# Kernel tuning notes

Hardware: AMD Instinct MI355X
Metric: run time of the kernel (lower is better)

The kernel has to match this reference:

```python
import jax, jax.numpy as jnp
import numpy as np

B, SQ, SKV, DIN, DOUT = 8, 2048, 2048, 512, 512

def setup_inputs() -> dict:
    key = jax.random.key(0)
    ks = jax.random.split(key, 8)
    s = 1.0 / np.sqrt(DIN)
    return {
        "query": jax.random.normal(ks[0], (B, SQ, DIN), jnp.float32),
        "key": jax.random.normal(ks[1], (B, SKV, DIN), jnp.float32),
        "value": jax.random.normal(ks[2], (B, SKV, DIN), jnp.float32),
        "offset": jax.random.normal(ks[3], (B, SQ, DIN), jnp.float32),
        "Wq": jax.random.normal(ks[4], (DIN, DOUT), jnp.float32) * s,
        "Wk": jax.random.normal(ks[5], (DIN, DOUT), jnp.float32) * s,
        "Wv": jax.random.normal(ks[6], (DIN, DOUT), jnp.float32) * s,
        "Woff": jax.random.normal(ks[7], (DIN, SKV), jnp.float32) * s,
    }

def reference(query, key, value, offset, Wq, Wk, Wv, Woff):
    # q/k/v projections (nn.Linear, no bias)
    q = jnp.einsum("bqi,io->bqo", query, Wq)   # [B,SQ,DOUT]
    k = jnp.einsum("bki,io->bko", key, Wk)     # [B,SKV,DOUT]
    v = jnp.einsum("bki,io->bko", value, Wv)   # [B,SKV,DOUT]
    scale = 1.0 / jnp.sqrt(jnp.asarray(q.shape[-1], jnp.float32))
    scores = jnp.einsum("bqd,bkd->bqk", q, k) * scale  # [B,SQ,SKV]
    attn = jax.nn.softmax(scores, axis=-1)
    # offset bias is added AFTER softmax (no renormalization), per original
    attn = attn + jnp.einsum("bqi,ik->bqk", offset, Woff)
    return jnp.einsum("bqk,bkd->bqd", attn, v)  # [B,SQ,DOUT]
```

## Files before the change

kernel.cpp:

```cpp
#include <hip/hip_runtime.h>
#include <hip/hip_bf16.h>
#include <stdint.h>

typedef __bf16 bf16;
typedef unsigned char u8;
typedef bf16 bf16x4_t __attribute__((ext_vector_type(4)));
typedef bf16 bf16x8_t __attribute__((ext_vector_type(8)));
typedef float floatx4_t __attribute__((ext_vector_type(4)));

#define NB 8
#define SQ 2048
#define SKV 2048
#define DIN 512
#define DOUT 512

#define SCORE_SCALE 0.0027621358640099513f
#define P_STORE_SCALE 0.0625f
#define P_UNDO_SCALE 16.0f

__device__ __forceinline__ void load_lds16(const void* g, void* l) {
    __builtin_amdgcn_global_load_lds(
        (const __attribute__((address_space(1))) unsigned int*)g,
        (__attribute__((address_space(3))) unsigned int*)l, 16, 0, 0);
}

__device__ __forceinline__ u8 to_fp8(float f) {
    int v = __builtin_amdgcn_cvt_pk_fp8_f32(f, 0.f, 0, false);
    return (u8)(v & 0xff);
}
__device__ __forceinline__ unsigned int pack_fp8x4(float a, float b, float c, float d) {
    int lo = __builtin_amdgcn_cvt_pk_fp8_f32(a, b, 0, false);
    int all = __builtin_amdgcn_cvt_pk_fp8_f32(c, d, lo, true);
    return (unsigned int)all;
}

__device__ __forceinline__ int swz_off(int row, int col) {
    return (col & ~63) | ((((col >> 4) & 3) ^ ((row >> 1) & 3)) << 4) | (col & 15);
}

__device__ __forceinline__ void cast_bf16_16B(const float4* s4, u8* d, int t, int rs) {
    const long long b0 = (long long)t * 16;
    const int row = (int)(b0 >> rs);
    const int cb = (int)(b0 & ((1 << rs) - 1));
    float4 f0 = s4[t * 2], f1 = s4[t * 2 + 1];
    bf16x8_t o = { (bf16)f0.x, (bf16)f0.y, (bf16)f0.z, (bf16)f0.w,
                   (bf16)f1.x, (bf16)f1.y, (bf16)f1.z, (bf16)f1.w };
    *(bf16x8_t*)&d[((long long)row << rs) + swz_off(row, cb)] = o;
}

struct CastArgs {
    const float* src[3];
    void* dst[3];
    int n[3];
    int mode[3];
    int rowshift[3];
};
__global__ __launch_bounds__(256) void cast_many(CastArgs a) {
    const int z = blockIdx.z;
    const int t = blockIdx.x * 256 + threadIdx.x;
    if (t >= a.n[z]) return;
    const float4* s4 = (const float4*)a.src[z];
    u8* d = (u8*)a.dst[z];
    const int rs = a.rowshift[z];
    if (a.mode[z] == 1) {
        const long long b0 = (long long)t * 16;
        const int row = (int)(b0 >> rs);
        const int cb = (int)(b0 & ((1 << rs) - 1));
        u8* dst = &d[((long long)row << rs) + swz_off(row, cb)];
        float4 f[4];
#pragma unroll
        for (int k = 0; k < 4; ++k) f[k] = s4[t * 4 + k];
        uint4 o;
        o.x = pack_fp8x4(f[0].x, f[0].y, f[0].z, f[0].w);
        o.y = pack_fp8x4(f[1].x, f[1].y, f[1].z, f[1].w);
        o.z = pack_fp8x4(f[2].x, f[2].y, f[2].z, f[2].w);
        o.w = pack_fp8x4(f[3].x, f[3].y, f[3].z, f[3].w);
        *(uint4*)dst = o;
    } else {
        cast_bf16_16B(s4, d, t, rs);
    }
}

struct TWArgs { const float* src[3]; void* dst[3]; };
__global__ void transpose_w(TWArgs a) {
    __shared__ float t[32][33];
    const float* src = a.src[blockIdx.z];
    int tx = threadIdx.x, ty = threadIdx.y;
    int x0 = blockIdx.x * 32, y0 = blockIdx.y * 32;
#pragma unroll
    for (int j = 0; j < 4; ++j)
        t[ty + 8 * j][tx] = src[(y0 + ty + 8 * j) * DIN + x0 + tx];
    __syncthreads();
    if (blockIdx.z <= 1) {
        u8* d8 = (u8*)a.dst[blockIdx.z];
#pragma unroll
        for (int j = 0; j < 4; ++j) {
            int row = x0 + ty + 8 * j, col = y0 + tx;
            d8[row * 512 + swz_off(row, col)] = to_fp8(t[tx][ty + 8 * j] * 4.0f);
        }
    } else {
        u8* db = (u8*)a.dst[2];
#pragma unroll
        for (int j = 0; j < 4; ++j) {
            int row = x0 + ty + 8 * j, cb = (y0 + tx) * 2;
            *(bf16*)&db[(long long)row * 1024 + swz_off(row, cb)] = (bf16)t[tx][ty + 8 * j];
        }
    }
}

__device__ __forceinline__ void gemm_mainloop(
    floatx4_t (&acc)[4][4], const bf16* __restrict__ Ap, const bf16* __restrict__ Bp,
    int lda, int ldb, int K, bf16* As, bf16* Bs, int wave, int lane)
{
    const int wm = (wave & 1) * 64, wn = (wave >> 1) * 64;
    const int lm = lane & 15, quad = lane >> 4;
    const int srow = lane >> 2, scol = (lane & 3) * 8;
    const int key = (lm >> 1) & 3;

    auto STAGE = [&](int buf, int k0) {
#pragma unroll
        for (int t = 0; t < 2; ++t) {
            const int r0 = (wave * 2 + t) * 16;
            load_lds16(Ap + (long long)(r0 + srow) * lda + (k0 + scol),
                       &As[buf * 4096 + r0 * 32]);
            load_lds16(Bp + (long long)(r0 + srow) * ldb + (k0 + scol),
                       &Bs[buf * 4096 + r0 * 32]);
        }
    };

    STAGE(0, 0);
    __syncthreads();
    int cur = 0;
    for (int k0 = 0; k0 < K; k0 += 32) {
        if (k0 + 32 < K) STAGE(cur ^ 1, k0 + 32);
        bf16x8_t af[4], bfr[4];
#pragma unroll
        for (int i = 0; i < 4; ++i)
            af[i] = *(const bf16x8_t*)&As[cur * 4096 + (wm + i * 16 + lm) * 32 + (quad ^ key) * 8];
#pragma unroll
        for (int i = 0; i < 4; ++i)
            bfr[i] = *(const bf16x8_t*)&Bs[cur * 4096 + (wn + i * 16 + lm) * 32 + (quad ^ key) * 8];
#pragma unroll
        for (int i = 0; i < 4; ++i)
#pragma unroll
            for (int j = 0; j < 4; ++j)
                acc[i][j] = __builtin_amdgcn_mfma_f32_16x16x32_bf16(af[i], bfr[j], acc[i][j], 0, 0, 0);
        __syncthreads();
        cur ^= 1;
    }
}

__device__ __forceinline__ void gemm_mainloop_fp8(
    floatx4_t (&acc)[4][4], const u8* __restrict__ Ap, const u8* __restrict__ Bp,
    int lda, int ldb, int K, u8* As, u8* Bs, int wave, int lane)
{
    const int wm = (wave & 1) * 64, wn = (wave >> 1) * 64;
    const int lm = lane & 15, quad = lane >> 4;
    const int srow = lane >> 2, scol = (lane & 3) * 16;
    const int key = (lm >> 1) & 3;
    const int inner = (quad & 1) * 8;
    const int gh = quad >> 1;

    auto STAGE = [&](int buf, int k0) {
#pragma unroll
        for (int t = 0; t < 2; ++t) {
            const int r0 = (wave * 2 + t) * 16;
            load_lds16(Ap + (long long)(r0 + srow) * lda + k0 + scol, &As[buf * 8192 + r0 * 64]);
            load_lds16(Bp + (long long)(r0 + srow) * ldb + k0 + scol, &Bs[buf * 8192 + r0 * 64]);
        }
    };

    STAGE(0, 0);
    __syncthreads();
    int cur = 0;
    for (int k0 = 0; k0 < K; k0 += 64) {
        if (k0 + 64 < K) STAGE(cur ^ 1, k0 + 64);
#pragma unroll
        for (int p = 0; p < 2; ++p) {
            const int gL = p * 2 + gh;
            const int koff = ((gL ^ key) << 4) + inner;
            long long a[4], b[4];
#pragma unroll
            for (int i = 0; i < 4; ++i)
                a[i] = *(const long long*)&As[cur * 8192 + (wm + i * 16 + lm) * 64 + koff];
#pragma unroll
            for (int i = 0; i < 4; ++i)
                b[i] = *(const long long*)&Bs[cur * 8192 + (wn + i * 16 + lm) * 64 + koff];
#pragma unroll
            for (int i = 0; i < 4; ++i)
#pragma unroll
                for (int j = 0; j < 4; ++j)
                    acc[i][j] = __builtin_amdgcn_mfma_f32_16x16x32_fp8_fp8(a[i], b[j], acc[i][j], 0, 0, 0);
        }
        __syncthreads();
        cur ^= 1;
    }
}

__global__ __launch_bounds__(256) void proj_gemm(
    const u8* __restrict__ query8, const u8* __restrict__ key8,
    const u8* __restrict__ WqT8, const u8* __restrict__ WkT8,
    u8* __restrict__ Qb8, u8* __restrict__ Kb8,
    const bf16* __restrict__ valueb, const bf16* __restrict__ WvT,
    bf16* __restrict__ VT, u8* __restrict__ VT8,
    const float* __restrict__ Woff, bf16* __restrict__ Woffb)
{
    __shared__ __align__(16) u8 smem[32768];
    const int tid = threadIdx.x;
    const int id = blockIdx.x;
    if (id >= 1536) {
        const int t = (id - 1536) * 256 + tid;
        cast_bf16_16B((const float4*)Woff, (u8*)Woffb, t, 12);
        return;
    }
    const int wave = tid >> 6, lane = tid & 63;
    const int wm = (wave & 1) * 64, wn = (wave >> 1) * 64;
    const int lm = lane & 15, quad = lane >> 4;

    floatx4_t acc[4][4];
#pragma unroll
    for (int i = 0; i < 4; ++i)
#pragma unroll
        for (int j = 0; j < 4; ++j) acc[i][j] = 0.0f;

    if (id < 1024) {
        const int xcd = id & 7, t = id >> 3, m = t & 3;
        const int gg = xcd + 8 * (t >> 2);
        const int y = gg & 127, z = gg >> 7;
        const u8* Ap = (z ? key8 : query8) + (long long)y * 128 * DIN;
        const u8* Bp = (z ? WkT8 : WqT8) + (long long)m * 128 * DIN;
        gemm_mainloop_fp8(acc, Ap, Bp, DIN, DIN, DIN, smem, smem + 16384, wave, lane);
        u8* C = z ? Kb8 : Qb8;
#pragma unroll
        for (int i = 0; i < 4; ++i)
#pragma unroll
            for (int j = 0; j < 4; ++j) {
                const int row0 = y * 128 + wm + i * 16 + quad * 4;
                const int col = m * 128 + wn + j * 16 + lm;
#pragma unroll
                for (int r = 0; r < 4; ++r)
                    C[(long long)(row0 + r) * DOUT + swz_off(row0 + r, col)] = to_fp8(acc[i][j][r]);
            }
    } else {
        const int id2 = id - 1024;
        const int z = id2 & 7, r2 = id2 >> 3;
        const int ym = r2 & 3, xn = r2 >> 2;
        const bf16* Ap = WvT + (long long)ym * 128 * DIN;
        const bf16* Bp = valueb + (long long)z * (SKV * DIN) + (long long)xn * 128 * DIN;
        gemm_mainloop(acc, Ap, Bp, DIN, DIN, DIN, (bf16*)smem, (bf16*)(smem + 16384), wave, lane);
        u8* C = (u8*)(VT + (long long)z * (DOUT * SKV));
        u8* C8 = VT8 + (long long)z * (DOUT * SKV);
#pragma unroll
        for (int i = 0; i < 4; ++i)
#pragma unroll
            for (int j = 0; j < 4; ++j) {
                const int row0 = ym * 128 + wm + i * 16 + quad * 4;
                const int col = xn * 128 + wn + j * 16 + lm;
#pragma unroll
                for (int r = 0; r < 4; ++r) {
                    float v = acc[i][j][r];
                    const int rr = row0 + r;
                    *(bf16*)&C[(long long)rr * (SKV * 2) + swz_off(rr, col * 2)] = (bf16)v;
                    C8[(long long)rr * SKV + swz_off(rr, col)] = to_fp8(v);
                }
            }
    }
}

__global__ __launch_bounds__(256) void g_gemm(
    const bf16* __restrict__ VT, const bf16* __restrict__ Woffb,
    float* __restrict__ G32a, float* __restrict__ G32b,
    const float* __restrict__ offset, bf16* __restrict__ offsetb,
    float* __restrict__ lbuf)
{
    __shared__ __align__(16) u8 smem[32768];
    const int tid = threadIdx.x;
    const int id = blockIdx.x;
    if (id >= 4352) {
        float4* d4 = (float4*)lbuf;
        const int t = (id - 4352) * 256 + tid;
#pragma unroll
        for (int k = 0; k < 4; ++k)
            d4[t * 4 + k] = make_float4(0.f, 0.f, 0.f, 0.f);
        return;
    }
    if (id >= 256) {
        const int t = (id - 256) * 256 + tid;
        cast_bf16_16B((const float4*)offset, (u8*)offsetb, t, 10);
        return;
    }
    const int wave = tid >> 6, lane = tid & 63;
    const int z = id & 7, h = (id >> 3) & 1, x = (id >> 4) & 3, y = (id >> 6) & 3;

    floatx4_t acc[4][4];
#pragma unroll
    for (int i = 0; i < 4; ++i)
#pragma unroll
        for (int j = 0; j < 4; ++j) acc[i][j] = 0.0f;

    const bf16* Ap = VT + (long long)z * (DOUT * SKV) + (long long)y * 128 * SKV + h * 1024;
    const bf16* Bp = Woffb + (long long)x * 128 * SKV + h * 1024;
    gemm_mainloop(acc, Ap, Bp, SKV, SKV, 1024, (bf16*)smem, (bf16*)(smem + 16384), wave, lane);

    const int wm = (wave & 1) * 64, wn = (wave >> 1) * 64;
    const int lm = lane & 15, quad = lane >> 4;
    float* C = (h ? G32b : G32a) + (long long)z * (DOUT * DIN);
#pragma unroll
    for (int i = 0; i < 4; ++i)
#pragma unroll
        for (int j = 0; j < 4; ++j) {
            const int row0 = y * 128 + wm + i * 16 + quad * 4;
            const int col = x * 128 + wn + j * 16 + lm;
#pragma unroll
            for (int r = 0; r < 4; ++r)
                C[(long long)(row0 + r) * DIN + col] = acc[i][j][r];
        }
}

__global__ __launch_bounds__(256) void s_gemm_exp(
    const u8* __restrict__ Qb8, const u8* __restrict__ Kb8,
    u8* __restrict__ expS8, float* __restrict__ l,
    const float* __restrict__ G32a, const float* __restrict__ G32b,
    bf16* __restrict__ Gb)
{
    __shared__ __align__(16) u8 smem[32768];
    const int tid = threadIdx.x;
    const int id = blockIdx.x;
    if (id >= 2048) {
        const int base = (id - 2048) * 256 + tid;
        const float4* A4 = (const float4*)G32a;
        const float4* B4 = (const float4*)G32b;
        u8* O = (u8*)Gb;
#pragma unroll 4
        for (int t = 0; t < 32; ++t) {
            const int idx = base + t * 16384;
            float4 a = A4[idx], b = B4[idx];
            bf16x4_t o = { (bf16)(a.x + b.x), (bf16)(a.y + b.y),
                           (bf16)(a.z + b.z), (bf16)(a.w + b.w) };
            const long long boff = (long long)idx * 8;
            const int row = (int)(boff >> 10);
            const int cb = (int)(boff & 1023);
            *(bf16x4_t*)&O[((long long)row << 10) + swz_off(row, cb)] = o;
        }
        return;
    }
    const int wave = tid >> 6, lane = tid & 63;
    const int z = id & 7, x = (id >> 3) & 15, y = (id >> 3) >> 4;

    floatx4_t acc[4][4];
#pragma unroll
    for (int i = 0; i < 4; ++i)
#pragma unroll
        for (int j = 0; j < 4; ++j) acc[i][j] = 0.0f;

    const u8* Ap = Qb8 + ((long long)z * SQ + (long long)y * 128) * DOUT;
    const u8* Bp = Kb8 + ((long long)z * SKV + (long long)x * 128) * DOUT;
    gemm_mainloop_fp8(acc, Ap, Bp, DOUT, DOUT, DOUT, smem, smem + 16384, wave, lane);

    const int wm = (wave & 1) * 64, wn = (wave >> 1) * 64;
    const int lm = lane & 15, quad = lane >> 4;
    u8* C = expS8 + (long long)z * SQ * SKV;
    const long long grow0 = (long long)z * SQ + (long long)y * 128;
#pragma unroll
    for (int i = 0; i < 4; ++i) {
        float rs[4] = {0.f, 0.f, 0.f, 0.f};
#pragma unroll
        for (int j = 0; j < 4; ++j) {
            const int row0 = y * 128 + wm + i * 16 + quad * 4;
            const int col = x * 128 + wn + j * 16 + lm;
#pragma unroll
            for (int r = 0; r < 4; ++r) {
                float e = __expf(acc[i][j][r] * SCORE_SCALE);
                rs[r] += e;
                C[(long long)(row0 + r) * SKV + swz_off(row0 + r, col)] = to_fp8(e * P_STORE_SCALE);
            }
        }
#pragma unroll
        for (int r = 0; r < 4; ++r) {
            float v = rs[r];
            v += __shfl_xor(v, 1, 64);
            v += __shfl_xor(v, 2, 64);
            v += __shfl_xor(v, 4, 64);
            v += __shfl_xor(v, 8, 64);
            if (lm == 0)
                atomicAdd(&l[grow0 + wm + i * 16 + quad * 4 + r], v);
        }
    }
}

__global__ __launch_bounds__(256) void out_gemm(
    const u8* __restrict__ expS8, const u8* __restrict__ VT8,
    const bf16* __restrict__ offb, const bf16* __restrict__ Gb,
    const float* __restrict__ l, float* __restrict__ out)
{
    __shared__ __align__(16) u8 smem[32768];
    const int tid = threadIdx.x;
    const int wave = tid >> 6, lane = tid & 63;
    const int id = blockIdx.x;
    const int z = id & 7, x = (id >> 3) & 3, y = (id >> 3) >> 2;

    floatx4_t acc[4][4];
#pragma unroll
    for (int i = 0; i < 4; ++i)
#pragma unroll
        for (int j = 0; j < 4; ++j) acc[i][j] = 0.0f;

    {
        const u8* Ap = expS8 + (long long)z * SQ * SKV + (long long)y * 128 * SKV;
        const u8* Bp = VT8 + (long long)z * DOUT * SKV + (long long)x * 128 * SKV;
        gemm_mainloop_fp8(acc, Ap, Bp, SKV, SKV, SKV, smem, smem + 16384, wave, lane);
    }

    const int wm = (wave & 1) * 64, wn = (wave >> 1) * 64;
    const int lm = lane & 15, quad = lane >> 4;
    const long long grow0 = (long long)z * SQ + (long long)y * 128;

#pragma unroll
    for (int i = 0; i < 4; ++i)
#pragma unroll
        for (int r = 0; r < 4; ++r) {
            const float inv = P_UNDO_SCALE / l[grow0 + wm + i * 16 + quad * 4 + r];
#pragma unroll
            for (int j = 0; j < 4; ++j) acc[i][j][r] *= inv;
        }

    {
        const bf16* Ap = offb + grow0 * DIN;
        const bf16* Bp = Gb + (long long)z * DOUT * DIN + (long long)x * 128 * DIN;
        gemm_mainloop(acc, Ap, Bp, DIN, DIN, DIN, (bf16*)smem, (bf16*)(smem + 16384), wave, lane);
    }

#pragma unroll
    for (int i = 0; i < 4; ++i)
#pragma unroll
        for (int j = 0; j < 4; ++j) {
            const long long row0 = grow0 + wm + i * 16 + quad * 4;
            const int col = x * 128 + wn + j * 16 + lm;
#pragma unroll
            for (int r = 0; r < 4; ++r)
                out[(row0 + r) * DOUT + col] = acc[i][j][r];
        }
}

extern "C" void kernel_launch(void* const* d_in, const int* in_sizes, int n_in,
                              void* d_out, int out_size, void* d_ws, size_t ws_size,
                              hipStream_t stream) {
    const float* query = (const float*)d_in[0];
    const float* key_ = (const float*)d_in[1];
    const float* value = (const float*)d_in[2];
    const float* offset = (const float*)d_in[3];
    const float* Wq = (const float*)d_in[4];
    const float* Wk = (const float*)d_in[5];
    const float* Wv = (const float*)d_in[6];
    const float* Woff = (const float*)d_in[7];
    float* out = (float*)d_out;

    char* ws = (char*)d_ws;
    const long long NE = (long long)NB * SQ * DIN;
    const long long MB = 1048576;

    u8* query8   = (u8*)(ws + 0 * MB);
    u8* key8     = (u8*)(ws + 8 * MB);
    bf16* valueb = (bf16*)(ws + 16 * MB);
    bf16* offsetb= (bf16*)(ws + 32 * MB);
    u8* Qb8      = (u8*)(ws + 48 * MB);
    u8* Kb8      = (u8*)(ws + 56 * MB);
    bf16* VT     = (bf16*)(ws + 64 * MB);
    u8* VT8      = (u8*)(ws + 80 * MB);
    float* G32a  = (float*)(ws + 88 * MB);
    float* G32b  = (float*)(ws + 96 * MB);
    bf16* Gb     = (bf16*)(ws + 104 * MB);
    u8* WqT8     = (u8*)(ws + 108 * MB);
    u8* WkT8     = (u8*)(ws + 108 * MB + 262144);
    bf16* WvT    = (bf16*)(ws + 108 * MB + 524288);
    bf16* Woffb  = (bf16*)(ws + 109 * MB);
    float* lbuf  = (float*)(ws + 111 * MB);
    u8* expS8    = (u8*)(ws + 112 * MB);

    CastArgs ca;
    ca.src[0] = query; ca.dst[0] = query8; ca.n[0] = (int)(NE / 16); ca.mode[0] = 1; ca.rowshift[0] = 9;
    ca.src[1] = key_;  ca.dst[1] = key8;   ca.n[1] = (int)(NE / 16); ca.mode[1] = 1; ca.rowshift[1] = 9;
    ca.src[2] = value; ca.dst[2] = valueb; ca.n[2] = (int)(NE / 8);  ca.mode[2] = 0; ca.rowshift[2] = 10;
    cast_many<<<dim3(4096, 1, 3), 256, 0, stream>>>(ca);

    TWArgs tw;
    tw.src[0] = Wq; tw.src[1] = Wk; tw.src[2] = Wv;
    tw.dst[0] = WqT8; tw.dst[1] = WkT8; tw.dst[2] = WvT;
    transpose_w<<<dim3(16, 16, 3), dim3(32, 8), 0, stream>>>(tw);

    proj_gemm<<<dim3(2048), 256, 0, stream>>>(query8, key8, WqT8, WkT8, Qb8, Kb8,
                                              valueb, WvT, VT, VT8, Woff, Woffb);

    g_gemm<<<dim3(4356), 256, 0, stream>>>(VT, Woffb, G32a, G32b, offset, offsetb, lbuf);

    s_gemm_exp<<<dim3(2112), 256, 0, stream>>>(Qb8, Kb8, expS8, lbuf, G32a, G32b, Gb);

    out_gemm<<<dim3(512), 256, 0, stream>>>(expS8, VT8, offsetb, Gb, lbuf, out);
}
```

Baseline: 306.4 us.

## Triple-buffer GEMM mainloops with explicit vmcnt waits and raw barriers

Both the bf16 and fp8 GEMM mainloops now keep three LDS stages in flight instead of two, prefetching two k-steps ahead. The blanket __syncthreads is replaced by explicit s_waitcnt vmcnt counts plus s_barrier with sched_barrier fences. The goal is to hide global-to-LDS load latency behind the MFMA work. In exchange, shared memory per block grows from 32 KB to 48 KB, which may reduce occupancy, and correctness now depends on the hand-counted vmcnt values.

```diff
diff --git a/kernel.cpp b/kernel.cpp
--- a/kernel.cpp
+++ b/kernel.cpp
@@ -22,6 +22,20 @@
     __builtin_amdgcn_global_load_lds(
         (const __attribute__((address_space(1))) unsigned int*)g,
         (__attribute__((address_space(3))) unsigned int*)l, 16, 0, 0);
+}
+
+__device__ __forceinline__ void wait_vm4() {
+    asm volatile("s_waitcnt vmcnt(4)" ::: "memory");
+    __builtin_amdgcn_sched_barrier(0);
+}
+__device__ __forceinline__ void wait_vm0() {
+    asm volatile("s_waitcnt vmcnt(0)" ::: "memory");
+    __builtin_amdgcn_sched_barrier(0);
+}
+__device__ __forceinline__ void hard_barrier() {
+    __builtin_amdgcn_sched_barrier(0);
+    __builtin_amdgcn_s_barrier();
+    __builtin_amdgcn_sched_barrier(0);
 }
 
 __device__ __forceinline__ u8 to_fp8(float f) {
@@ -128,11 +142,14 @@
         }
     };
 
+    const int nsteps = K >> 5;
     STAGE(0, 0);
-    __syncthreads();
-    int cur = 0;
-    for (int k0 = 0; k0 < K; k0 += 32) {
-        if (k0 + 32 < K) STAGE(cur ^ 1, k0 + 32);
+    STAGE(1, 32);
+    wait_vm4();
+    hard_barrier();
+    int cur = 0, stg = 2;
+    for (int s = 0; s < nsteps; ++s) {
+        if (s + 2 < nsteps) STAGE(stg, (s + 2) << 5);
         bf16x8_t af[4], bfr[4];
 #pragma unroll
         for (int i = 0; i < 4; ++i)
@@ -145,8 +162,12 @@
 #pragma unroll
             for (int j = 0; j < 4; ++j)
                 acc[i][j] = __builtin_amdgcn_mfma_f32_16x16x32_bf16(af[i], bfr[j], acc[i][j], 0, 0, 0);
-        __syncthreads();
-        cur ^= 1;
+        if (s + 1 < nsteps) {
+            if (s + 2 < nsteps) wait_vm4(); else wait_vm0();
+        }
+        hard_barrier();
+        cur = (cur == 2) ? 0 : cur + 1;
+        stg = (stg == 2) ? 0 : stg + 1;
     }
 }
 
@@ -170,11 +191,14 @@
         }
     };
 
+    const int nsteps = K >> 6;
     STAGE(0, 0);
-    __syncthreads();
-    int cur = 0;
-    for (int k0 = 0; k0 < K; k0 += 64) {
-        if (k0 + 64 < K) STAGE(cur ^ 1, k0 + 64);
+    STAGE(1, 64);
+    wait_vm4();
+    hard_barrier();
+    int cur = 0, stg = 2;
+    for (int s = 0; s < nsteps; ++s) {
+        if (s + 2 < nsteps) STAGE(stg, (s + 2) << 6);
 #pragma unroll
         for (int p = 0; p < 2; ++p) {
             const int gL = p * 2 + gh;
@@ -192,8 +216,12 @@
                 for (int j = 0; j < 4; ++j)
                     acc[i][j] = __builtin_amdgcn_mfma_f32_16x16x32_fp8_fp8(a[i], b[j], acc[i][j], 0, 0, 0);
         }
-        __syncthreads();
-        cur ^= 1;
+        if (s + 1 < nsteps) {
+            if (s + 2 < nsteps) wait_vm4(); else wait_vm0();
+        }
+        hard_barrier();
+        cur = (cur == 2) ? 0 : cur + 1;
+        stg = (stg == 2) ? 0 : stg + 1;
     }
 }
 
@@ -205,7 +233,7 @@
     bf16* __restrict__ VT, u8* __restrict__ VT8,
     const float* __restrict__ Woff, bf16* __restrict__ Woffb)
 {
-    __shared__ __align__(16) u8 smem[32768];
+    __shared__ __align__(16) u8 smem[49152];
     const int tid = threadIdx.x;
     const int id = blockIdx.x;
     if (id >= 1536) {
@@ -229,7 +257,7 @@
         const int y = gg & 127, z = gg >> 7;
         const u8* Ap = (z ? key8 : query8) + (long long)y * 128 * DIN;
         const u8* Bp = (z ? WkT8 : WqT8) + (long long)m * 128 * DIN;
-        gemm_mainloop_fp8(acc, Ap, Bp, DIN, DIN, DIN, smem, smem + 16384, wave, lane);
+        gemm_mainloop_fp8(acc, Ap, Bp, DIN, DIN, DIN, smem, smem + 24576, wave, lane);
         u8* C = z ? Kb8 : Qb8;
 #pragma unroll
         for (int i = 0; i < 4; ++i)
@@ -247,7 +275,7 @@
         const int ym = r2 & 3, xn = r2 >> 2;
         const bf16* Ap = WvT + (long long)ym * 128 * DIN;
         const bf16* Bp = valueb + (long long)z * (SKV * DIN) + (long long)xn * 128 * DIN;
-        gemm_mainloop(acc, Ap, Bp, DIN, DIN, DIN, (bf16*)smem, (bf16*)(smem + 16384), wave, lane);
+        gemm_mainloop(acc, Ap, Bp, DIN, DIN, DIN, (bf16*)smem, (bf16*)(smem + 24576), wave, lane);
         u8* C = (u8*)(VT + (long long)z * (DOUT * SKV));
         u8* C8 = VT8 + (long long)z * (DOUT * SKV);
 #pragma unroll
@@ -273,7 +301,7 @@
     const float* __restrict__ offset, bf16* __restrict__ offsetb,
     float* __restrict__ lbuf)
 {
-    __shared__ __align__(16) u8 smem[32768];
+    __shared__ __align__(16) u8 smem[49152];
     const int tid = threadIdx.x;
     const int id = blockIdx.x;
     if (id >= 4352) {
@@ -300,7 +328,7 @@
 
     const bf16* Ap = VT + (long long)z * (DOUT * SKV) + (long long)y * 128 * SKV + h * 1024;
     const bf16* Bp = Woffb + (long long)x * 128 * SKV + h * 1024;
-    gemm_mainloop(acc, Ap, Bp, SKV, SKV, 1024, (bf16*)smem, (bf16*)(smem + 16384), wave, lane);
+    gemm_mainloop(acc, Ap, Bp, SKV, SKV, 1024, (bf16*)smem, (bf16*)(smem + 24576), wave, lane);
 
     const int wm = (wave & 1) * 64, wn = (wave >> 1) * 64;
     const int lm = lane & 15, quad = lane >> 4;
@@ -323,7 +351,7 @@
     const float* __restrict__ G32a, const float* __restrict__ G32b,
     bf16* __restrict__ Gb)
 {
-    __shared__ __align__(16) u8 smem[32768];
+    __shared__ __align__(16) u8 smem[49152];
     const int tid = threadIdx.x;
     const int id = blockIdx.x;
     if (id >= 2048) {
@@ -355,7 +383,7 @@
 
     const u8* Ap = Qb8 + ((long long)z * SQ + (long long)y * 128) * DOUT;
     const u8* Bp = Kb8 + ((long long)z * SKV + (long long)x * 128) * DOUT;
-    gemm_mainloop_fp8(acc, Ap, Bp, DOUT, DOUT, DOUT, smem, smem + 16384, wave, lane);
+    gemm_mainloop_fp8(acc, Ap, Bp, DOUT, DOUT, DOUT, smem, smem + 24576, wave, lane);
 
     const int wm = (wave & 1) * 64, wn = (wave >> 1) * 64;
     const int lm = lane & 15, quad = lane >> 4;
@@ -393,7 +421,7 @@
     const bf16* __restrict__ offb, const bf16* __restrict__ Gb,
     const float* __restrict__ l, float* __restrict__ out)
 {
-    __shared__ __align__(16) u8 smem[32768];
+    __shared__ __align__(16) u8 smem[49152];
     const int tid = threadIdx.x;
     const int wave = tid >> 6, lane = tid & 63;
     const int id = blockIdx.x;
@@ -408,7 +436,7 @@
     {
         const u8* Ap = expS8 + (long long)z * SQ * SKV + (long long)y * 128 * SKV;
         const u8* Bp = VT8 + (long long)z * DOUT * SKV + (long long)x * 128 * SKV;
-        gemm_mainloop_fp8(acc, Ap, Bp, SKV, SKV, SKV, smem, smem + 16384, wave, lane);
+        gemm_mainloop_fp8(acc, Ap, Bp, SKV, SKV, SKV, smem, smem + 24576, wave, lane);
     }
 
     const int wm = (wave & 1) * 64, wn = (wave >> 1) * 64;
@@ -427,7 +455,7 @@
     {
         const bf16* Ap = offb + grow0 * DIN;
         const bf16* Bp = Gb + (long long)z * DOUT * DIN + (long long)x * 128 * DIN;
-        gemm_mainloop(acc, Ap, Bp, DIN, DIN, DIN, (bf16*)smem, (bf16*)(smem + 16384), wave, lane);
+        gemm_mainloop(acc, Ap, Bp, DIN, DIN, DIN, (bf16*)smem, (bf16*)(smem + 24576), wave, lane);
     }
 
 #pragma unroll
```

Result: no change. 301.4 us (-1.6%).

## Use per-wave private LDS staging to drop block barriers in GEMM mainloops

Applied to the files above, without the earlier changes.

Replaces the cooperative block-wide LDS staging (with __syncthreads each k-step) by per-wave private LDS regions, where each wave loads only its own 64-row A and B slices. A two-deep prefetch is added, synchronised with explicit s_waitcnt vmcnt/lgkmcnt and sched_barrier instead of block barriers, and shared memory grows to 64KB per block. The intent is to remove barrier stalls and let waves run independently. In exchange, A and B tiles are loaded twice across waves, which raises global/L2 traffic, and the larger LDS footprint lowers occupancy.

```diff
diff --git a/kernel.cpp b/kernel.cpp
--- a/kernel.cpp
+++ b/kernel.cpp
@@ -108,7 +108,133 @@
     }
 }
 
-__device__ __forceinline__ void gemm_mainloop(
+
+template<int K>
+__device__ __forceinline__ void gemm_pw_fp8(
+    floatx4_t (&acc)[4][4], const u8* __restrict__ Ap, const u8* __restrict__ Bp,
+    int lda, int ldb, u8* lds, int wave, int lane)
+{
+    const int wm = (wave & 1) * 64, wn = (wave >> 1) * 64;
+    const int lm = lane & 15, quad = lane >> 4;
+    const int srow = lane >> 2, scol = (lane & 3) * 16;
+    const int key = (lm >> 1) & 3;
+    const int inner = (quad & 1) * 8;
+    const int gh = quad >> 1;
+
+    const u8* ap[4]; const u8* bp[4];
+#pragma unroll
+    for (int t = 0; t < 4; ++t) {
+        ap[t] = Ap + (long long)(wm + t * 16 + srow) * lda + scol;
+        bp[t] = Bp + (long long)(wn + t * 16 + srow) * ldb + scol;
+    }
+    auto STAGE = [&](int buf, int k0) {
+#pragma unroll
+        for (int t = 0; t < 4; ++t)
+            load_lds16(ap[t] + k0, lds + buf * 8192 + t * 1024);
+#pragma unroll
+        for (int t = 0; t < 4; ++t)
+            load_lds16(bp[t] + k0, lds + buf * 8192 + 4096 + t * 1024);
+    };
+    constexpr int nsteps = K / 64;
+    STAGE(0, 0);
+    STAGE(1, 64);
+    asm volatile("s_waitcnt vmcnt(8)" ::: "memory");
+    __builtin_amdgcn_sched_barrier(0);
+    int cur = 0;
+#pragma unroll 2
+    for (int s = 0; s < nsteps; ++s) {
+        const u8* A0 = lds + cur * 8192;
+        const u8* B0 = A0 + 4096;
+        long long a[2][4], b[2][4];
+#pragma unroll
+        for (int p = 0; p < 2; ++p) {
+            const int koff = (((p * 2 + gh) ^ key) << 4) + inner;
+#pragma unroll
+            for (int i = 0; i < 4; ++i) {
+                a[p][i] = *(const long long*)&A0[(i * 16 + lm) * 64 + koff];
+                b[p][i] = *(const long long*)&B0[(i * 16 + lm) * 64 + koff];
+            }
+        }
+        asm volatile("s_waitcnt lgkmcnt(0)" ::: "memory");
+        __builtin_amdgcn_sched_barrier(0);
+        if (s + 2 < nsteps) STAGE(cur, (s + 2) * 64);
+#pragma unroll
+        for (int p = 0; p < 2; ++p)
+#pragma unroll
+            for (int i = 0; i < 4; ++i)
+#pragma unroll
+                for (int j = 0; j < 4; ++j)
+                    acc[i][j] = __builtin_amdgcn_mfma_f32_16x16x32_fp8_fp8(a[p][i], b[p][j], acc[i][j], 0, 0, 0);
+        if (s + 1 < nsteps) {
+            if (s + 2 < nsteps) { asm volatile("s_waitcnt vmcnt(8)" ::: "memory"); }
+            else                { asm volatile("s_waitcnt vmcnt(0)" ::: "memory"); }
+            __builtin_amdgcn_sched_barrier(0);
+        }
+        cur ^= 1;
+    }
+}
+
+template<int K>
+__device__ __forceinline__ void gemm_pw_bf16(
+    floatx4_t (&acc)[4][4], const bf16* __restrict__ Apb, const bf16* __restrict__ Bpb,
+    int lda, int ldb, u8* lds, int wave, int lane)
+{
+    const u8* Ap = (const u8*)Apb; const u8* Bp = (const u8*)Bpb;
+    const long long ldaB = (long long)lda * 2, ldbB = (long long)ldb * 2;
+    const int wm = (wave & 1) * 64, wn = (wave >> 1) * 64;
+    const int lm = lane & 15, quad = lane >> 4;
+    const int srow = lane >> 2, scol = (lane & 3) * 16;
+    const int key = (lm >> 1) & 3;
+
+    const u8* ap[4]; const u8* bp[4];
+#pragma unroll
+    for (int t = 0; t < 4; ++t) {
+        ap[t] = Ap + (long long)(wm + t * 16 + srow) * ldaB + scol;
+        bp[t] = Bp + (long long)(wn + t * 16 + srow) * ldbB + scol;
+    }
+    auto STAGE = [&](int buf, int k0b) {
+#pragma unroll
+        for (int t = 0; t < 4; ++t)
+            load_lds16(ap[t] + k0b, lds + buf * 8192 + t * 1024);
+#pragma unroll
+        for (int t = 0; t < 4; ++t)
+            load_lds16(bp[t] + k0b, lds + buf * 8192 + 4096 + t * 1024);
+    };
+    constexpr int nsteps = K / 32;
+    STAGE(0, 0);
+    STAGE(1, 64);
+    asm volatile("s_waitcnt vmcnt(8)" ::: "memory");
+    __builtin_amdgcn_sched_barrier(0);
+    int cur = 0;
+#pragma unroll 2
+    for (int s = 0; s < nsteps; ++s) {
+        const u8* A0 = lds + cur * 8192;
+        const u8* B0 = A0 + 4096;
+        const int koff = ((quad ^ key) << 4);
+        bf16x8_t af[4], bfr[4];
+#pragma unroll
+        for (int i = 0; i < 4; ++i) {
+            af[i] = *(const bf16x8_t*)&A0[(i * 16 + lm) * 64 + koff];
+            bfr[i] = *(const bf16x8_t*)&B0[(i * 16 + lm) * 64 + koff];
+        }
+        asm volatile("s_waitcnt lgkmcnt(0)" ::: "memory");
+        __builtin_amdgcn_sched_barrier(0);
+        if (s + 2 < nsteps) STAGE(cur, (s + 2) * 64);
+#pragma unroll
+        for (int i = 0; i < 4; ++i)
+#pragma unroll
+            for (int j = 0; j < 4; ++j)
+                acc[i][j] = __builtin_amdgcn_mfma_f32_16x16x32_bf16(af[i], bfr[j], acc[i][j], 0, 0, 0);
+        if (s + 1 < nsteps) {
+            if (s + 2 < nsteps) { asm volatile("s_waitcnt vmcnt(8)" ::: "memory"); }
+            else                { asm volatile("s_waitcnt vmcnt(0)" ::: "memory"); }
+            __builtin_amdgcn_sched_barrier(0);
+        }
+        cur ^= 1;
+    }
+}
+
+__device__ __forceinline__ void gemm_mainloop_coop(
     floatx4_t (&acc)[4][4], const bf16* __restrict__ Ap, const bf16* __restrict__ Bp,
     int lda, int ldb, int K, bf16* As, bf16* Bs, int wave, int lane)
 {
@@ -145,53 +271,6 @@
 #pragma unroll
             for (int j = 0; j < 4; ++j)
                 acc[i][j] = __builtin_amdgcn_mfma_f32_16x16x32_bf16(af[i], bfr[j], acc[i][j], 0, 0, 0);
-        __syncthreads();
-        cur ^= 1;
-    }
-}
-
-__device__ __forceinline__ void gemm_mainloop_fp8(
-    floatx4_t (&acc)[4][4], const u8* __restrict__ Ap, const u8* __restrict__ Bp,
-    int lda, int ldb, int K, u8* As, u8* Bs, int wave, int lane)
-{
-    const int wm = (wave & 1) * 64, wn = (wave >> 1) * 64;
-    const int lm = lane & 15, quad = lane >> 4;
-    const int srow = lane >> 2, scol = (lane & 3) * 16;
-    const int key = (lm >> 1) & 3;
-    const int inner = (quad & 1) * 8;
-    const int gh = quad >> 1;
-
-    auto STAGE = [&](int buf, int k0) {
-#pragma unroll
-        for (int t = 0; t < 2; ++t) {
-            const int r0 = (wave * 2 + t) * 16;
-            load_lds16(Ap + (long long)(r0 + srow) * lda + k0 + scol, &As[buf * 8192 + r0 * 64]);
-            load_lds16(Bp + (long long)(r0 + srow) * ldb + k0 + scol, &Bs[buf * 8192 + r0 * 64]);
-        }
-    };
-
-    STAGE(0, 0);
-    __syncthreads();
-    int cur = 0;
-    for (int k0 = 0; k0 < K; k0 += 64) {
-        if (k0 + 64 < K) STAGE(cur ^ 1, k0 + 64);
-#pragma unroll
-        for (int p = 0; p < 2; ++p) {
-            const int gL = p * 2 + gh;
-            const int koff = ((gL ^ key) << 4) + inner;
-            long long a[4], b[4];
-#pragma unroll
-            for (int i = 0; i < 4; ++i)
-                a[i] = *(const long long*)&As[cur * 8192 + (wm + i * 16 + lm) * 64 + koff];
-#pragma unroll
-            for (int i = 0; i < 4; ++i)
-                b[i] = *(const long long*)&Bs[cur * 8192 + (wn + i * 16 + lm) * 64 + koff];
-#pragma unroll
-            for (int i = 0; i < 4; ++i)
-#pragma unroll
-                for (int j = 0; j < 4; ++j)
-                    acc[i][j] = __builtin_amdgcn_mfma_f32_16x16x32_fp8_fp8(a[i], b[j], acc[i][j], 0, 0, 0);
-        }
         __syncthreads();
         cur ^= 1;
     }
@@ -205,7 +284,7 @@
     bf16* __restrict__ VT, u8* __restrict__ VT8,
     const float* __restrict__ Woff, bf16* __restrict__ Woffb)
 {
-    __shared__ __align__(16) u8 smem[32768];
+    __shared__ __align__(16) u8 smem[65536];
     const int tid = threadIdx.x;
     const int id = blockIdx.x;
     if (id >= 1536) {
@@ -216,6 +295,7 @@
     const int wave = tid >> 6, lane = tid & 63;
     const int wm = (wave & 1) * 64, wn = (wave >> 1) * 64;
     const int lm = lane & 15, quad = lane >> 4;
+    u8* mylds = smem + wave * 16384;
 
     floatx4_t acc[4][4];
 #pragma unroll
@@ -229,7 +309,7 @@
         const int y = gg & 127, z = gg >> 7;
         const u8* Ap = (z ? key8 : query8) + (long long)y * 128 * DIN;
         const u8* Bp = (z ? WkT8 : WqT8) + (long long)m * 128 * DIN;
-        gemm_mainloop_fp8(acc, Ap, Bp, DIN, DIN, DIN, smem, smem + 16384, wave, lane);
+        gemm_pw_fp8<DIN>(acc, Ap, Bp, DIN, DIN, mylds, wave, lane);
         u8* C = z ? Kb8 : Qb8;
 #pragma unroll
         for (int i = 0; i < 4; ++i)
@@ -247,7 +327,7 @@
         const int ym = r2 & 3, xn = r2 >> 2;
         const bf16* Ap = WvT + (long long)ym * 128 * DIN;
         const bf16* Bp = valueb + (long long)z * (SKV * DIN) + (long long)xn * 128 * DIN;
-        gemm_mainloop(acc, Ap, Bp, DIN, DIN, DIN, (bf16*)smem, (bf16*)(smem + 16384), wave, lane);
+        gemm_pw_bf16<DIN>(acc, Ap, Bp, DIN, DIN, mylds, wave, lane);
         u8* C = (u8*)(VT + (long long)z * (DOUT * SKV));
         u8* C8 = VT8 + (long long)z * (DOUT * SKV);
 #pragma unroll
@@ -300,7 +380,7 @@
 
     const bf16* Ap = VT + (long long)z * (DOUT * SKV) + (long long)y * 128 * SKV + h * 1024;
     const bf16* Bp = Woffb + (long long)x * 128 * SKV + h * 1024;
-    gemm_mainloop(acc, Ap, Bp, SKV, SKV, 1024, (bf16*)smem, (bf16*)(smem + 16384), wave, lane);
+    gemm_mainloop_coop(acc, Ap, Bp, SKV, SKV, 1024, (bf16*)smem, (bf16*)(smem + 16384), wave, lane);
 
     const int wm = (wave & 1) * 64, wn = (wave >> 1) * 64;
     const int lm = lane & 15, quad = lane >> 4;
@@ -323,7 +403,7 @@
     const float* __restrict__ G32a, const float* __restrict__ G32b,
     bf16* __restrict__ Gb)
 {
-    __shared__ __align__(16) u8 smem[32768];
+    __shared__ __align__(16) u8 smem[65536];
     const int tid = threadIdx.x;
     const int id = blockIdx.x;
     if (id >= 2048) {
@@ -346,6 +426,7 @@
     }
     const int wave = tid >> 6, lane = tid & 63;
     const int z = id & 7, x = (id >> 3) & 15, y = (id >> 3) >> 4;
+    u8* mylds = smem + wave * 16384;
 
     floatx4_t acc[4][4];
 #pragma unroll
@@ -355,7 +436,7 @@
 
     const u8* Ap = Qb8 + ((long long)z * SQ + (long long)y * 128) * DOUT;
     const u8* Bp = Kb8 + ((long long)z * SKV + (long long)x * 128) * DOUT;
-    gemm_mainloop_fp8(acc, Ap, Bp, DOUT, DOUT, DOUT, smem, smem + 16384, wave, lane);
+    gemm_pw_fp8<DOUT>(acc, Ap, Bp, DOUT, DOUT, mylds, wave, lane);
 
     const int wm = (wave & 1) * 64, wn = (wave >> 1) * 64;
     const int lm = lane & 15, quad = lane >> 4;
@@ -393,11 +474,12 @@
     const bf16* __restrict__ offb, const bf16* __restrict__ Gb,
     const float* __restrict__ l, float* __restrict__ out)
 {
-    __shared__ __align__(16) u8 smem[32768];
+    __shared__ __align__(16) u8 smem[65536];
     const int tid = threadIdx.x;
     const int wave = tid >> 6, lane = tid & 63;
     const int id = blockIdx.x;
     const int z = id & 7, x = (id >> 3) & 3, y = (id >> 3) >> 2;
+    u8* mylds = smem + wave * 16384;
 
     floatx4_t acc[4][4];
 #pragma unroll
@@ -408,7 +490,7 @@
     {
         const u8* Ap = expS8 + (long long)z * SQ * SKV + (long long)y * 128 * SKV;
         const u8* Bp = VT8 + (long long)z * DOUT * SKV + (long long)x * 128 * SKV;
-        gemm_mainloop_fp8(acc, Ap, Bp, SKV, SKV, SKV, smem, smem + 16384, wave, lane);
+        gemm_pw_fp8<SKV>(acc, Ap, Bp, SKV, SKV, mylds, wave, lane);
     }
 
     const int wm = (wave & 1) * 64, wn = (wave >> 1) * 64;
@@ -427,7 +509,7 @@
     {
         const bf16* Ap = offb + grow0 * DIN;
         const bf16* Bp = Gb + (long long)z * DOUT * DIN + (long long)x * 128 * DIN;
-        gemm_mainloop(acc, Ap, Bp, DIN, DIN, DIN, (bf16*)smem, (bf16*)(smem + 16384), wave, lane);
+        gemm_pw_bf16<DIN>(acc, Ap, Bp, DIN, DIN, mylds, wave, lane);
     }
 
 #pragma unroll
```

Result: slower. 326.6 us (+6.6%).
